# Kernel tuning notes

Measured on AMD Instinct MI355X. Metric: run time of the kernel, lower is better.

## Reference

```python
import jax, jax.numpy as jnp
import numpy as np

C = 256
CQ = C // 8  # query/key channels


def setup_inputs() -> dict:
    key = jax.random.key(0)
    ks = jax.random.split(key, 8)
    B, H, W = 4, 64, 64
    x = jax.random.normal(ks[0], (B, C, H, W), dtype=jnp.float32)
    mask = jax.random.uniform(ks[1], (B, 1, H, W), dtype=jnp.float32)
    # 1x1 conv weights stored as [out_ch, in_ch] (kernel_size=1)
    s = 1.0 / np.sqrt(C)
    Wq = jax.random.uniform(ks[2], (CQ, C), dtype=jnp.float32, minval=-s, maxval=s)
    bq = jax.random.uniform(ks[3], (CQ,), dtype=jnp.float32, minval=-s, maxval=s)
    Wk = jax.random.uniform(ks[4], (CQ, C), dtype=jnp.float32, minval=-s, maxval=s)
    bk = jax.random.uniform(ks[5], (CQ,), dtype=jnp.float32, minval=-s, maxval=s)
    Wv = jax.random.uniform(ks[6], (C, C), dtype=jnp.float32, minval=-s, maxval=s)
    bv = jax.random.uniform(ks[7], (C,), dtype=jnp.float32, minval=-s, maxval=s)
    gamma = jnp.ones((1,), dtype=jnp.float32)
    return {"x": x, "mask": mask, "Wq": Wq, "bq": bq, "Wk": Wk, "bk": bk,
            "Wv": Wv, "bv": bv, "gamma": gamma}


def reference(x, mask, Wq, bq, Wk, bk, Wv, bv, gamma):
    B, Cc, H, W = x.shape
    N = H * W
    xf = x.reshape(B, Cc, N)                  # [B, C, N]
    m = mask.reshape(B, 1, N)                 # [B, 1, N]
    # 1x1 convs == per-pixel linear maps over channels
    q = jnp.einsum('oc,bcn->bon', Wq, xf) + bq[None, :, None]  # [B, CQ, N]
    k = jnp.einsum('oc,bcn->bon', Wk, xf) + bk[None, :, None]  # [B, CQ, N]
    v = jnp.einsum('oc,bcn->bon', Wv, xf) + bv[None, :, None]  # [B, C,  N]
    q = q * m
    k = k * m
    energy = jnp.einsum('bci,bcj->bij', q, k)  # [B, N, N] (queries x keys)
    attn = jax.nn.softmax(energy, axis=-1)
    out = jnp.einsum('bcj,bij->bci', v, attn)  # [B, C, N]
    out = out.reshape(B, Cc, H, W)
    return gamma * out + x
```

## Files before the change

kernel.cpp:

```cpp
#include <hip/hip_runtime.h>
#include <math.h>

#define CC 256
#define NPIX 4096
#define BATCH 4
#define LOG2E 1.4426950408889634f

typedef __attribute__((ext_vector_type(8)))  short short8;
typedef __attribute__((ext_vector_type(8)))  int   int32x8;
typedef __attribute__((ext_vector_type(16))) float f32x16;

union FragU { short8 v; short s[8]; unsigned u[4]; uint2 d[2]; };
union V8  { uint4 q[2]; int32x8 iv; };
union B8  { unsigned u[8]; int32x8 iv; };

__device__ inline unsigned pkbf(float a, float b) {
    unsigned x = __float_as_uint(a), y = __float_as_uint(b);
    x = (x + 0x7FFFu + ((x >> 16) & 1u)) >> 16;
    y = (y + 0x7FFFu + ((y >> 16) & 1u)) & 0xFFFF0000u;
    return x | y;
}
__device__ inline unsigned short bf1(float a) {
    unsigned x = __float_as_uint(a);
    return (unsigned short)((x + 0x7FFFu + ((x >> 16) & 1u)) >> 16);
}
__device__ inline float ex2(float x) { return __builtin_amdgcn_exp2f(x); }
__device__ inline unsigned pk4fp8(float a, float b, float c, float d) {
    int r = __builtin_amdgcn_cvt_pk_fp8_f32(a, b, 0, false);
    r = __builtin_amdgcn_cvt_pk_fp8_f32(c, d, r, true);
    return (unsigned)r;
}
__device__ inline f32x16 zero16() {
    f32x16 v;
    #pragma unroll
    for (int i = 0; i < 16; ++i) v[i] = 0.0f;
    return v;
}
__device__ inline f32x16 mfma32(short8 a, short8 b, f32x16 c) {
    return __builtin_amdgcn_mfma_f32_32x32x16_bf16(a, b, c, 0, 0, 0);
}
__device__ inline f32x16 mfma64s(int32x8 a, int32x8 b, f32x16 c) {
    return __builtin_amdgcn_mfma_scale_f32_32x32x64_f8f6f4(
        a, b, c, 0 , 0 , 0, 0x7F, 0, 0x7F);
}

__global__ __launch_bounds__(256, 2) void prep_w(
    const float* __restrict__ Wq, const float* __restrict__ Wk,
    const float* __restrict__ Wv, unsigned short* __restrict__ Wfrag)
{
    const int t = threadIdx.x;
    const int wb = blockIdx.x;
    const int l = t & 63, rr = t >> 6;
    #pragma unroll
    for (int e = 0; e < 4; ++e) {
        int gs = wb * 4 + e;
        int g = gs >> 4, s = gs & 15;
        const float* src; float scale = 1.0f; int oc0 = 0;
        if (g == 0)      { src = Wq; scale = LOG2E; }
        else if (g == 1) { src = Wk; }
        else             { src = Wv; oc0 = (g - 2) * 32; }
        int row = oc0 + (l & 31);
        int kb2 = 16 * s + 8 * (l >> 5) + rr * 2;
        float v0 = src[(size_t)row * CC + kb2] * scale;
        float v1 = src[(size_t)row * CC + kb2 + 1] * scale;
        *(unsigned*)(Wfrag + (size_t)(gs * 64 + l) * 8 + rr * 2) = pkbf(v0, v1);
    }
}

__global__ __launch_bounds__(640, 2) void proj_mfma(
    const float* __restrict__ x, const unsigned short* __restrict__ Wfrag,
    const float* __restrict__ mask,
    const float* __restrict__ bq, const float* __restrict__ bk,
    const float* __restrict__ bv,
    unsigned short* __restrict__ qT, unsigned short* __restrict__ kT,
    unsigned char* __restrict__ vI)
{
    __shared__ unsigned short xls[64 * 260];
    const int t = threadIdx.x;
    const int w = t >> 6, l = t & 63, L = l & 31, h = l >> 5;
    const int bid = blockIdx.x;
    const int b    = (bid >> 1) & 3;
    const int u    = ((bid >> 3) << 1) | (bid & 1);
    const int p0   = u * 64;
    const int ocg  = w;

    if (t < 512) {
        const int pg = t & 15;
        const int cb = (t >> 4) * 2;
        const float* xb = x + (size_t)b * CC * NPIX + p0 + pg * 4;
        #pragma unroll
        for (int k = 0; k < 4; ++k) {
            int c = cb + 64 * k;
            float4 v0 = *(const float4*)(xb + (size_t)c * NPIX);
            float4 v1 = *(const float4*)(xb + (size_t)(c + 1) * NPIX);
            *(unsigned*)&xls[(pg * 4 + 0) * 260 + c] = pkbf(v0.x, v1.x);
            *(unsigned*)&xls[(pg * 4 + 1) * 260 + c] = pkbf(v0.y, v1.y);
            *(unsigned*)&xls[(pg * 4 + 2) * 260 + c] = pkbf(v0.z, v1.z);
            *(unsigned*)&xls[(pg * 4 + 3) * 260 + c] = pkbf(v0.w, v1.w);
        }
    }

    FragU wf[16];
    const unsigned short* wp = Wfrag + (size_t)(ocg * 16 * 64 + l) * 8;
    #pragma unroll
    for (int s = 0; s < 16; ++s) wf[s].v = *(const short8*)(wp + s * 512);

    float bcol;
    if (ocg == 0)      bcol = bq[L] * LOG2E;
    else if (ocg == 1) bcol = bk[L];
    else               bcol = bv[(ocg - 2) * 32 + L];
    const float* mb = mask + (size_t)b * NPIX;
    __syncthreads();

    #pragma unroll
    for (int mt = 0; mt < 2; ++mt) {
        const int pp = 32 * mt;
        f32x16 acc = zero16();
        #pragma unroll
        for (int s = 0; s < 16; ++s) {
            FragU af;
            const unsigned short* ap = &xls[(pp + L) * 260 + 16 * s + 8 * h];
            af.d[0] = *(const uint2*)(ap);
            af.d[1] = *(const uint2*)(ap + 4);
            acc = mfma32(af.v, wf[s].v, acc);
        }
        if (ocg < 2) {
            unsigned short* dst = (ocg ? kT : qT) + (size_t)b * NPIX * 32;
            #pragma unroll
            for (int r = 0; r < 16; ++r) {
                int prow = (r & 3) + 8 * (r >> 2) + 4 * h;
                float mv = mb[p0 + pp + prow];
                dst[(size_t)(p0 + pp + prow) * 32 + L] = bf1((acc[r] + bcol) * mv);
            }
        } else {
            const int cg = ocg - 2;
            const int jb32 = p0 + pp;
            unsigned char* dst = vI + (size_t)b * (1 << 20)
                + (size_t)(jb32 >> 6) * 16384 + cg * 2048
                + (((jb32 >> 5) & 1) * 32 + L) * 32 + 4 * h;
            #pragma unroll
            for (int m = 0; m < 4; ++m) {
                unsigned pk = pk4fp8(acc[4*m]   + bcol, acc[4*m+1] + bcol,
                                     acc[4*m+2] + bcol, acc[4*m+3] + bcol);
                *(unsigned*)(dst + 8 * m) = pk;
            }
        }
    }
}

__global__ __launch_bounds__(256, 2) void attn_mfma(
    const unsigned short* __restrict__ qT, const unsigned short* __restrict__ kT,
    const unsigned char* __restrict__ vI, const float* __restrict__ x,
    const float* __restrict__ gamma, float* __restrict__ out)
{
    __shared__ float mls[4][32];
    __shared__ float lls[2][4][32];
    __shared__ float obuf[4][2048];

    const int t = threadIdx.x;
    const int w = t >> 6, l = t & 63, L = l & 31, h = l >> 5;
    const int bid = blockIdx.x;
    const int b  = (bid >> 1) & 3;
    const int it = (bid >> 3) * 2 + (bid & 1);
    const int i0 = it * 32;

    const unsigned short* qrow = qT + ((size_t)b * NPIX + i0 + L) * 32 + 8 * h;
    short8 qf0 = *(const short8*)(qrow);
    short8 qf1 = *(const short8*)(qrow + 16);

    const int jbase = w * 1024;
    const unsigned char* kp = (const unsigned char*)kT
        + (size_t)b * NPIX * 64 + (size_t)jbase * 64 + (size_t)L * 64 + 16 * h;
    short8 ka0 = *(const short8*)(kp);
    short8 ka1 = *(const short8*)(kp + 32);
    short8 kb0 = *(const short8*)(kp + 2048);
    short8 kb1 = *(const short8*)(kp + 2080);
    kp += 4096;
    const unsigned char* vp = vI + (size_t)b * (1 << 20)
        + (size_t)(jbase >> 6) * 16384 + (size_t)l * 32;

    f32x16 acc[8];
    #pragma unroll
    for (int cg = 0; cg < 8; ++cg) acc[cg] = zero16();
    float m_run = -INFINITY, l_run = 0.0f;
    bool warm = false;

    f32x16 s0 = zero16(), s1 = zero16();
    __builtin_amdgcn_s_setprio(1);
    s0 = mfma32(ka0, qf0, s0);
    s0 = mfma32(ka1, qf1, s0);
    s1 = mfma32(kb0, qf0, s1);
    s1 = mfma32(kb1, qf1, s1);
    __builtin_amdgcn_s_setprio(0);

    for (int itr = 0; itr < 16; ++itr) {
        ka0 = *(const short8*)(kp);
        ka1 = *(const short8*)(kp + 32);
        kb0 = *(const short8*)(kp + 2048);
        kb1 = *(const short8*)(kp + 2080);
        kp += 4096;

        V8 vv[4];
        #pragma unroll
        for (int cg = 0; cg < 4; ++cg) {
            vv[cg].q[0] = *(const uint4*)(vp + cg * 2048);
            vv[cg].q[1] = *(const uint4*)(vp + cg * 2048 + 16);
        }

        float t0 = fmaxf(fmaxf(s0[0],  s0[4]),  s0[8]);
        float t1 = fmaxf(fmaxf(s0[1],  s0[5]),  s0[9]);
        float t2 = fmaxf(fmaxf(s0[2],  s0[6]),  s0[10]);
        float t3 = fmaxf(fmaxf(s0[3],  s0[7]),  s0[11]);
        t0 = fmaxf(fmaxf(t0, s0[12]), s1[0]);
        t1 = fmaxf(fmaxf(t1, s0[13]), s1[1]);
        t2 = fmaxf(fmaxf(t2, s0[14]), s1[2]);
        t3 = fmaxf(fmaxf(t3, s0[15]), s1[3]);
        t0 = fmaxf(fmaxf(t0, s1[4]),  s1[8]);
        t1 = fmaxf(fmaxf(t1, s1[5]),  s1[9]);
        t2 = fmaxf(fmaxf(t2, s1[6]),  s1[10]);
        t3 = fmaxf(fmaxf(t3, s1[7]),  s1[11]);
        t0 = fmaxf(t0, s1[12]);
        t1 = fmaxf(t1, s1[13]);
        t2 = fmaxf(t2, s1[14]);
        t3 = fmaxf(t3, s1[15]);
        float tmax = fmaxf(fmaxf(fmaxf(t0, t1), t2), t3);
        tmax = fmaxf(tmax, __shfl_xor(tmax, 32));

        if (__ballot(tmax > m_run + 8.0f)) {
            float m_new = fmaxf(m_run, tmax);
            if (warm) {
                float alpha = ex2(m_run - m_new);
                l_run *= alpha;
                #pragma unroll
                for (int cg = 0; cg < 8; ++cg)
                    #pragma unroll
                    for (int r = 0; r < 16; ++r) acc[cg][r] *= alpha;
            }
            m_run = m_new;
            warm = true;
        }

        float z0 = 0, z1 = 0, z2 = 0, z3 = 0;
        #pragma unroll
        for (int r = 0; r < 16; r += 4) {
            s0[r]   = ex2(s0[r]   - m_run); z0 += s0[r];
            s0[r+1] = ex2(s0[r+1] - m_run); z1 += s0[r+1];
            s0[r+2] = ex2(s0[r+2] - m_run); z2 += s0[r+2];
            s0[r+3] = ex2(s0[r+3] - m_run); z3 += s0[r+3];
        }
        #pragma unroll
        for (int r = 0; r < 16; r += 4) {
            s1[r]   = ex2(s1[r]   - m_run); z0 += s1[r];
            s1[r+1] = ex2(s1[r+1] - m_run); z1 += s1[r+1];
            s1[r+2] = ex2(s1[r+2] - m_run); z2 += s1[r+2];
            s1[r+3] = ex2(s1[r+3] - m_run); z3 += s1[r+3];
        }
        l_run += (z0 + z1) + (z2 + z3);

        unsigned u0[4], u1[4], p0[4], p1[4];
        #pragma unroll
        for (int m = 0; m < 4; ++m) {
            u0[m] = pk4fp8(s0[4*m], s0[4*m+1], s0[4*m+2], s0[4*m+3]);
            u1[m] = pk4fp8(s1[4*m], s1[4*m+1], s1[4*m+2], s1[4*m+3]);
        }
        #pragma unroll
        for (int q = 0; q < 4; ++q) {
            p0[q] = (unsigned)__shfl_xor((int)u0[q], 32);
            p1[q] = (unsigned)__shfl_xor((int)u1[q], 32);
        }
        B8 bf;
        #pragma unroll
        for (int m = 0; m < 4; ++m) {
            unsigned oh = h ? u1[m] : u0[m];
            unsigned ph = h ? p1[m] : p0[m];
            bf.u[2*m]     = h ? ph : oh;
            bf.u[2*m + 1] = h ? oh : ph;
        }

        __builtin_amdgcn_s_setprio(1);
        s0 = mfma32(ka1, qf1, mfma32(ka0, qf0, zero16()));
        s1 = mfma32(kb1, qf1, mfma32(kb0, qf0, zero16()));

        #pragma unroll
        for (int cg = 0; cg < 4; ++cg) acc[cg] = mfma64s(vv[cg].iv, bf.iv, acc[cg]);
        #pragma unroll
        for (int cg = 0; cg < 4; ++cg) {
            vv[cg].q[0] = *(const uint4*)(vp + (cg + 4) * 2048);
            vv[cg].q[1] = *(const uint4*)(vp + (cg + 4) * 2048 + 16);
        }
        #pragma unroll
        for (int cg = 0; cg < 4; ++cg) acc[cg + 4] = mfma64s(vv[cg].iv, bf.iv, acc[cg + 4]);
        __builtin_amdgcn_s_setprio(0);
        vp += 16384;
    }

    if (h == 0) mls[w][L] = m_run;
    lls[h][w][L] = l_run;
    __syncthreads();
    float m0 = mls[0][L], m1 = mls[1][L], m2 = mls[2][L], m3 = mls[3][L];
    float ms = fmaxf(fmaxf(fmaxf(m0, m1), m2), m3);
    float f0 = ex2(m0 - ms), f1 = ex2(m1 - ms);
    float f2 = ex2(m2 - ms), f3 = ex2(m3 - ms);
    float lstar = f0 * (lls[0][0][L] + lls[1][0][L])
                + f1 * (lls[0][1][L] + lls[1][1][L])
                + f2 * (lls[0][2][L] + lls[1][2][L])
                + f3 * (lls[0][3][L] + lls[1][3][L]);
    const float scale = gamma[0] / lstar;
    const float g0 = scale * f0, g1 = scale * f1;
    const float g2 = scale * f2, g3 = scale * f3;

    const int ti = t & 31, trow = t >> 5;
    for (int ck = 0; ck < 4; ++ck) {
        #pragma unroll
        for (int half = 0; half < 2; ++half) {
            #pragma unroll
            for (int r = 0; r < 16; ++r) {
                int prow = (r & 3) + 8 * (r >> 2) + 4 * h;
                obuf[w][half * 1024 + prow * 32 + L] = acc[2 * ck + half][r];
            }
        }
        __syncthreads();
        #pragma unroll
        for (int rr = 0; rr < 8; ++rr) {
            int cr = trow + 8 * rr;
            int idx = cr * 32 + ti;
            float sum = g0 * obuf[0][idx] + g1 * obuf[1][idx]
                      + g2 * obuf[2][idx] + g3 * obuf[3][idx];
            size_t gi = ((size_t)b * CC + ck * 64 + cr) * NPIX + i0 + ti;
            out[gi] = sum + x[gi];
        }
        __syncthreads();
    }
}

extern "C" void kernel_launch(void* const* d_in, const int* in_sizes, int n_in,
                              void* d_out, int out_size, void* d_ws, size_t ws_size,
                              hipStream_t stream) {
    const float* x     = (const float*)d_in[0];
    const float* mask  = (const float*)d_in[1];
    const float* Wq    = (const float*)d_in[2];
    const float* bq    = (const float*)d_in[3];
    const float* Wk    = (const float*)d_in[4];
    const float* bk    = (const float*)d_in[5];
    const float* Wv    = (const float*)d_in[6];
    const float* bv    = (const float*)d_in[7];
    const float* gamma = (const float*)d_in[8];
    float* out = (float*)d_out;

    unsigned short* ws = (unsigned short*)d_ws;
    unsigned short* qT = ws;
    unsigned short* kT = qT + (size_t)BATCH * NPIX * 32;
    unsigned char*  vI = (unsigned char*)(kT + (size_t)BATCH * NPIX * 32);
    unsigned short* xpad = (unsigned short*)(vI + (size_t)BATCH * CC * NPIX);
    unsigned short* Wfrag = xpad + (size_t)BATCH * NPIX * 256;

    prep_w<<<40, 256, 0, stream>>>(Wq, Wk, Wv, Wfrag);
    proj_mfma<<<256, 640, 0, stream>>>(x, Wfrag, mask, bq, bk, bv, qT, kT, vI);
    attn_mfma<<<512, 256, 0, stream>>>(qT, kT, vI, x, gamma, out);
}
```

Baseline: 123.0 us.

## Merge two query tiles per 512-thread block sharing K/V streams in lockstep

Each attention block now runs 8 waves: two groups of four, each group handling its own 32-query tile while sweeping the same four key quarters. A barrier inside the key loop keeps the paired waves in step, so identical K and V loads from both groups can be served from cache. The grid is halved and the shared buffers for the softmax merge and output reduction are doubled. The cost is a per-iteration block barrier and a launch bound of 512 threads with 2 blocks per CU, which tightens the register budget and may cause spills of the large accumulator array.

Result: slower. 130.2 us (+5.8%).

```diff
diff --git a/kernel.cpp b/kernel.cpp
--- a/kernel.cpp
+++ b/kernel.cpp
@@ -148,27 +148,29 @@
     }
 }
 
-__global__ __launch_bounds__(256, 2) void attn_mfma(
+__global__ __launch_bounds__(512, 2) void attn_mfma(
     const unsigned short* __restrict__ qT, const unsigned short* __restrict__ kT,
     const unsigned char* __restrict__ vI, const float* __restrict__ x,
     const float* __restrict__ gamma, float* __restrict__ out)
 {
-    __shared__ float mls[4][32];
-    __shared__ float lls[2][4][32];
-    __shared__ float obuf[4][2048];
+    __shared__ float mls[8][32];
+    __shared__ float lls[2][8][32];
+    __shared__ float obuf[8][2048];
 
     const int t = threadIdx.x;
     const int w = t >> 6, l = t & 63, L = l & 31, h = l >> 5;
     const int bid = blockIdx.x;
-    const int b  = (bid >> 1) & 3;
-    const int it = (bid >> 3) * 2 + (bid & 1);
-    const int i0 = it * 32;
+    const int b    = (bid >> 1) & 3;
+    const int it64 = (bid >> 3) * 2 + (bid & 1);
+    const int pair = w >> 2;
+    const int jq   = w & 3;
+    const int i0   = it64 * 64 + pair * 32;
 
     const unsigned short* qrow = qT + ((size_t)b * NPIX + i0 + L) * 32 + 8 * h;
     short8 qf0 = *(const short8*)(qrow);
     short8 qf1 = *(const short8*)(qrow + 16);
 
-    const int jbase = w * 1024;
+    const int jbase = jq * 1024;
     const unsigned char* kp = (const unsigned char*)kT
         + (size_t)b * NPIX * 64 + (size_t)jbase * 64 + (size_t)L * 64 + 16 * h;
     short8 ka0 = *(const short8*)(kp);
@@ -206,6 +208,8 @@
             vv[cg].q[0] = *(const uint4*)(vp + cg * 2048);
             vv[cg].q[1] = *(const uint4*)(vp + cg * 2048 + 16);
         }
+
+        __syncthreads();
 
         float t0 = fmaxf(fmaxf(s0[0],  s0[4]),  s0[8]);
         float t1 = fmaxf(fmaxf(s0[1],  s0[5]),  s0[9]);
@@ -297,19 +301,21 @@
     if (h == 0) mls[w][L] = m_run;
     lls[h][w][L] = l_run;
     __syncthreads();
-    float m0 = mls[0][L], m1 = mls[1][L], m2 = mls[2][L], m3 = mls[3][L];
+    const int q4 = pair * 4;
+    float m0 = mls[q4 + 0][L], m1 = mls[q4 + 1][L];
+    float m2 = mls[q4 + 2][L], m3 = mls[q4 + 3][L];
     float ms = fmaxf(fmaxf(fmaxf(m0, m1), m2), m3);
     float f0 = ex2(m0 - ms), f1 = ex2(m1 - ms);
     float f2 = ex2(m2 - ms), f3 = ex2(m3 - ms);
-    float lstar = f0 * (lls[0][0][L] + lls[1][0][L])
-                + f1 * (lls[0][1][L] + lls[1][1][L])
-                + f2 * (lls[0][2][L] + lls[1][2][L])
-                + f3 * (lls[0][3][L] + lls[1][3][L]);
+    float lstar = f0 * (lls[0][q4 + 0][L] + lls[1][q4 + 0][L])
+                + f1 * (lls[0][q4 + 1][L] + lls[1][q4 + 1][L])
+                + f2 * (lls[0][q4 + 2][L] + lls[1][q4 + 2][L])
+                + f3 * (lls[0][q4 + 3][L] + lls[1][q4 + 3][L]);
     const float scale = gamma[0] / lstar;
     const float g0 = scale * f0, g1 = scale * f1;
     const float g2 = scale * f2, g3 = scale * f3;
 
-    const int ti = t & 31, trow = t >> 5;
+    const int ti = t & 31, trow = (t >> 5) & 7, quad = t >> 8;
     for (int ck = 0; ck < 4; ++ck) {
         #pragma unroll
         for (int half = 0; half < 2; ++half) {
@@ -324,9 +330,10 @@
         for (int rr = 0; rr < 8; ++rr) {
             int cr = trow + 8 * rr;
             int idx = cr * 32 + ti;
-            float sum = g0 * obuf[0][idx] + g1 * obuf[1][idx]
-                      + g2 * obuf[2][idx] + g3 * obuf[3][idx];
-            size_t gi = ((size_t)b * CC + ck * 64 + cr) * NPIX + i0 + ti;
+            float sum = g0 * obuf[quad * 4 + 0][idx] + g1 * obuf[quad * 4 + 1][idx]
+                      + g2 * obuf[quad * 4 + 2][idx] + g3 * obuf[quad * 4 + 3][idx];
+            size_t gi = ((size_t)b * CC + ck * 64 + cr) * NPIX
+                      + it64 * 64 + quad * 32 + ti;
             out[gi] = sum + x[gi];
         }
         __syncthreads();
@@ -356,5 +363,5 @@
 
     prep_w<<<40, 256, 0, stream>>>(Wq, Wk, Wv, Wfrag);
     proj_mfma<<<256, 640, 0, stream>>>(x, Wfrag, mask, bq, bk, bv, qT, kT, vI);
-    attn_mfma<<<512, 256, 0, stream>>>(qT, kT, vI, x, gamma, out);
-}
+    attn_mfma<<<256, 512, 0, stream>>>(qT, kT, vI, x, gamma, out);
+}
```
